# Performance work log

Hardware: AMD Instinct MI355X
Metric: run time of the kernel (lower is better)

## Reference

```python
import jax, jax.numpy as jnp
import numpy as np

D = 512
H = 8
HD = D // H
EPS = 1e-5
NEG_INF = -1e30


def _ln(x, g, b):
    mu = jnp.mean(x, axis=-1, keepdims=True)
    var = jnp.mean(jnp.square(x - mu), axis=-1, keepdims=True)
    return (x - mu) * jax.lax.rsqrt(var + EPS) * g + b


def setup_inputs() -> dict:
    key = jax.random.key(0)
    ks = jax.random.split(key, 8)
    V, M, S = 128, 128, 514  # seq includes 2 head tokens (cls+dist)
    inp = {
        "video_embeds": jax.random.normal(ks[0], (V, D), jnp.float32),
        "music_features": jax.random.normal(ks[1], (M, S, D), jnp.float32),
        "music_masks": jnp.ones((M, S - 2), jnp.int32),
    }
    wk = jax.random.split(ks[2], 5)
    for name, k in zip(["Wq", "Wk", "Wv", "Wo", "Wl"], wk):
        inp[name] = jax.random.normal(k, (D, D), jnp.float32) * 0.02
    for name in ["bq", "bk", "bv", "bo", "bl"]:
        inp[name] = jnp.zeros((D,), jnp.float32)
    for name in ["g1", "g2", "g3"]:
        inp[name] = jnp.ones((D,), jnp.float32)
    for name in ["b1", "b2", "b3"]:
        inp[name] = jnp.zeros((D,), jnp.float32)
    return inp


def reference(video_embeds, music_features, music_masks,
              Wq, bq, Wk, bk, Wv, bv, Wo, bo, Wl, bl,
              g1, b1, g2, b2, g3, b3):
    # drop cls + dist tokens
    mf = music_features[:, 2:, :]  # (M, f, D)
    ve = _ln(video_embeds, g1, b1)  # (V, D)
    mf = _ln(mf, g1, b1)
    V = ve.shape[0]
    M, f, _ = mf.shape

    q = (ve @ Wq.T + bq).reshape(V, H, HD).transpose(1, 0, 2)        # (H, V, hd)
    k = (mf @ Wk.T + bk).reshape(M, f, H, HD).transpose(0, 2, 1, 3)  # (M, H, f, hd)
    v = (mf @ Wv.T + bv).reshape(M, f, H, HD).transpose(0, 2, 1, 3)  # (M, H, f, hd)

    logits = jnp.einsum('hvd,mhfd->vmhf', q, k) / np.sqrt(HD).astype(np.float32)
    mask = music_masks[None, :, None, :]  # (1, M, 1, f)
    logits = jnp.where(mask == 0, NEG_INF, logits)
    w = jax.nn.softmax(logits, axis=-1)
    attn = jnp.einsum('vmhf,mhfd->vmhd', w, v).reshape(V, M, D)
    attn = attn @ Wo.T + bo

    attn = _ln(attn, g2, b2)
    out = attn + (attn @ Wl.T + bl)  # dropout = identity in eval
    return _ln(out, g3, b3)
```

## Files before the change

kernel.cpp:

```cpp
#include <hip/hip_runtime.h>
#include <hip/hip_bf16.h>

typedef unsigned int uint;
typedef unsigned short ushort;
typedef __bf16 bf16;
typedef bf16 bf16x8 __attribute__((ext_vector_type(8)));
typedef float f32x4 __attribute__((ext_vector_type(4)));
typedef ushort ushort4v __attribute__((ext_vector_type(4)));

__device__ __forceinline__ float bf2f(ushort u) {
  union { uint u; float f; } v; v.u = ((uint)u) << 16; return v.f;
}
__device__ __forceinline__ ushort f2bf(float f) {
  union { float f; uint u; } v; v.f = f;
  uint u = v.u;
  uint r = (u + 0x7fffu + ((u >> 16) & 1u)) >> 16;
  return (ushort)r;
}

__device__ __forceinline__ void gl2lds16(const void* g, void* l) {
  __builtin_amdgcn_global_load_lds(
      (const __attribute__((address_space(1))) void*)g,
      (__attribute__((address_space(3))) void*)l, 16, 0, 0);
}

struct CastArgs {
  const float* s0; const float* s1; const float* s2; const float* s3; const float* s4;
  ushort* d0; ushort* d1; ushort* d2; ushort* d3; ushort* d4;
};
__global__ __launch_bounds__(256) void bfcast5(CastArgs a) {
  int t = blockIdx.x * 256 + threadIdx.x;
  int which = t >> 15;
  int e = (t & 32767) * 8;
  const float* s = which == 0 ? a.s0 : which == 1 ? a.s1 : which == 2 ? a.s2 : which == 3 ? a.s3 : a.s4;
  ushort*      d = which == 0 ? a.d0 : which == 1 ? a.d1 : which == 2 ? a.d2 : which == 3 ? a.d3 : a.d4;
  float4 v0 = *(const float4*)(s + e);
  float4 v1 = *(const float4*)(s + e + 4);
  uint4 o;
  o.x = (uint)f2bf(v0.x) | ((uint)f2bf(v0.y) << 16);
  o.y = (uint)f2bf(v0.z) | ((uint)f2bf(v0.w) << 16);
  o.z = (uint)f2bf(v1.x) | ((uint)f2bf(v1.y) << 16);
  o.w = (uint)f2bf(v1.z) | ((uint)f2bf(v1.w) << 16);
  *(uint4*)(d + e) = o;
}

__global__ __launch_bounds__(256) void ln512v(
    int mode, int nrows,
    const void* __restrict__ srcA, const void* __restrict__ srcB,
    const float* __restrict__ g, const float* __restrict__ b,
    void* __restrict__ dst)
{
  const int l = threadIdx.x & 63;
  const int nw = gridDim.x * 4;
  for (int row = blockIdx.x * 4 + (threadIdx.x >> 6); row < nrows; row += nw) {
    float x[8];
    if (mode <= 1) {
      const float* s;
      if (mode == 0) {
        s = (const float*)srcA + (size_t)row * 512;
      } else {
        int mm = row >> 9, fi = row & 511;
        s = (const float*)srcA + ((size_t)mm * 514 + 2 + fi) * 512;
      }
      float4 a0 = *(const float4*)(s + l * 4);
      float4 a1 = *(const float4*)(s + 256 + l * 4);
      x[0] = a0.x; x[1] = a0.y; x[2] = a0.z; x[3] = a0.w;
      x[4] = a1.x; x[5] = a1.y; x[6] = a1.z; x[7] = a1.w;
    } else if (mode == 2) {
      const ushort* s = (const ushort*)srcA + (size_t)row * 512;
      uint4 u = *(const uint4*)(s + l * 8);
      x[0] = bf2f((ushort)u.x); x[1] = bf2f((ushort)(u.x >> 16));
      x[2] = bf2f((ushort)u.y); x[3] = bf2f((ushort)(u.y >> 16));
      x[4] = bf2f((ushort)u.z); x[5] = bf2f((ushort)(u.z >> 16));
      x[6] = bf2f((ushort)u.w); x[7] = bf2f((ushort)(u.w >> 16));
    } else {
      const ushort* sa = (const ushort*)srcA + (size_t)row * 512;
      const ushort* sb = (const ushort*)srcB + (size_t)row * 512;
      uint4 ua = *(const uint4*)(sa + l * 8);
      uint4 ub = *(const uint4*)(sb + l * 8);
      x[0] = bf2f((ushort)ua.x) + bf2f((ushort)ub.x);
      x[1] = bf2f((ushort)(ua.x >> 16)) + bf2f((ushort)(ub.x >> 16));
      x[2] = bf2f((ushort)ua.y) + bf2f((ushort)ub.y);
      x[3] = bf2f((ushort)(ua.y >> 16)) + bf2f((ushort)(ub.y >> 16));
      x[4] = bf2f((ushort)ua.z) + bf2f((ushort)ub.z);
      x[5] = bf2f((ushort)(ua.z >> 16)) + bf2f((ushort)(ub.z >> 16));
      x[6] = bf2f((ushort)ua.w) + bf2f((ushort)ub.w);
      x[7] = bf2f((ushort)(ua.w >> 16)) + bf2f((ushort)(ub.w >> 16));
    }
    float sum = 0.f, sq = 0.f;
    #pragma unroll
    for (int j = 0; j < 8; ++j) { sum += x[j]; sq += x[j] * x[j]; }
    #pragma unroll
    for (int o = 1; o < 64; o <<= 1) {
      sum += __shfl_xor(sum, o);
      sq  += __shfl_xor(sq, o);
    }
    const float inv = 1.f / 512.f;
    float mu = sum * inv;
    float var = sq * inv - mu * mu;
    float rstd = rsqrtf(var + 1e-5f);

    float gv[8], bv[8];
    if (mode <= 1) {
      float4 g0 = *(const float4*)(g + l * 4);
      float4 g1 = *(const float4*)(g + 256 + l * 4);
      float4 b0 = *(const float4*)(b + l * 4);
      float4 b1 = *(const float4*)(b + 256 + l * 4);
      gv[0] = g0.x; gv[1] = g0.y; gv[2] = g0.z; gv[3] = g0.w;
      gv[4] = g1.x; gv[5] = g1.y; gv[6] = g1.z; gv[7] = g1.w;
      bv[0] = b0.x; bv[1] = b0.y; bv[2] = b0.z; bv[3] = b0.w;
      bv[4] = b1.x; bv[5] = b1.y; bv[6] = b1.z; bv[7] = b1.w;
    } else {
      float4 g0 = *(const float4*)(g + l * 8);
      float4 g1 = *(const float4*)(g + l * 8 + 4);
      float4 b0 = *(const float4*)(b + l * 8);
      float4 b1 = *(const float4*)(b + l * 8 + 4);
      gv[0] = g0.x; gv[1] = g0.y; gv[2] = g0.z; gv[3] = g0.w;
      gv[4] = g1.x; gv[5] = g1.y; gv[6] = g1.z; gv[7] = g1.w;
      bv[0] = b0.x; bv[1] = b0.y; bv[2] = b0.z; bv[3] = b0.w;
      bv[4] = b1.x; bv[5] = b1.y; bv[6] = b1.z; bv[7] = b1.w;
    }
    float y[8];
    #pragma unroll
    for (int j = 0; j < 8; ++j) y[j] = (x[j] - mu) * rstd * gv[j] + bv[j];

    if (mode <= 1) {
      ushort* d = (ushort*)dst + (size_t)row * 512;
      ushort4v p0, p1;
      #pragma unroll
      for (int j = 0; j < 4; ++j) { p0[j] = f2bf(y[j]); p1[j] = f2bf(y[4 + j]); }
      *(ushort4v*)(d + l * 4) = p0;
      *(ushort4v*)(d + 256 + l * 4) = p1;
    } else if (mode == 2) {
      ushort* d = (ushort*)dst + (size_t)row * 512;
      uint4 o;
      o.x = (uint)f2bf(y[0]) | ((uint)f2bf(y[1]) << 16);
      o.y = (uint)f2bf(y[2]) | ((uint)f2bf(y[3]) << 16);
      o.z = (uint)f2bf(y[4]) | ((uint)f2bf(y[5]) << 16);
      o.w = (uint)f2bf(y[6]) | ((uint)f2bf(y[7]) << 16);
      *(uint4*)(d + l * 8) = o;
    } else {
      float* d = (float*)dst + (size_t)row * 512;
      float4 o0, o1;
      o0.x = y[0]; o0.y = y[1]; o0.z = y[2]; o0.w = y[3];
      o1.x = y[4]; o1.y = y[5]; o1.z = y[6]; o1.w = y[7];
      *(float4*)(d + l * 8) = o0;
      *(float4*)(d + l * 8 + 4) = o1;
    }
  }
}

__global__ __launch_bounds__(512) void gemm512x(
    const ushort* __restrict__ A, const ushort* __restrict__ W,
    const float* __restrict__ bias, ushort* __restrict__ C,
    float scale, int vt_mode)
{
  __shared__ __align__(16) ushort As[128 * 64];
  __shared__ __align__(16) ushort Bs[256 * 64];
  const int tid = threadIdx.x;
  const int w = tid >> 6, l = tid & 63;
  const int lg = l >> 4, lr = l & 15;
  const int wr = w >> 2, wc = w & 3;

  int nwg = gridDim.x * gridDim.y;
  int bid = blockIdx.y * gridDim.x + blockIdx.x;
  if ((nwg & 7) == 0) bid = (bid & 7) * (nwg >> 3) + (bid >> 3);
  const int bx = bid % gridDim.x, by = bid / gridDim.x;
  const int row0 = by * 128, col0 = bx * 256;

  f32x4 acc[4][4];
  #pragma unroll
  for (int i = 0; i < 4; i++)
    #pragma unroll
    for (int j = 0; j < 4; j++) { f32x4 z = {0.f,0.f,0.f,0.f}; acc[i][j] = z; }

  for (int kk = 0; kk < 8; ++kk) {
    #pragma unroll
    for (int li = 0; li < 2; ++li) {
      int c = li * 512 + tid;
      int r = c >> 3, j = c & 7;
      gl2lds16(A + (size_t)(row0 + r) * 512 + kk * 64 + ((j ^ (r & 7)) * 8),
               As + (li * 512 + w * 64) * 8);
    }
    #pragma unroll
    for (int li = 0; li < 4; ++li) {
      int c = li * 512 + tid;
      int r = c >> 3, j = c & 7;
      gl2lds16(W + (size_t)(col0 + r) * 512 + kk * 64 + ((j ^ (r & 7)) * 8),
               Bs + (li * 512 + w * 64) * 8);
    }
    __syncthreads();
    #pragma unroll
    for (int ks = 0; ks < 2; ++ks) {
      bf16x8 af[4], bfr[4];
      #pragma unroll
      for (int mi = 0; mi < 4; ++mi) {
        int r = wr * 64 + mi * 16 + lr;
        af[mi] = *(const bf16x8*)(As + r * 64 + ((ks * 32 + lg * 8) ^ ((r & 7) * 8)));
      }
      #pragma unroll
      for (int ni = 0; ni < 4; ++ni) {
        int r = wc * 64 + ni * 16 + lr;
        bfr[ni] = *(const bf16x8*)(Bs + r * 64 + ((ks * 32 + lg * 8) ^ ((r & 7) * 8)));
      }
      #pragma unroll
      for (int mi = 0; mi < 4; ++mi)
        #pragma unroll
        for (int ni = 0; ni < 4; ++ni)
          acc[mi][ni] = __builtin_amdgcn_mfma_f32_16x16x32_bf16(af[mi], bfr[ni], acc[mi][ni], 0, 0, 0);
    }
    __syncthreads();
  }

  #pragma unroll
  for (int ni = 0; ni < 4; ++ni) {
    int cg = col0 + wc * 64 + ni * 16 + lr;
    float bc = bias[cg];
    #pragma unroll
    for (int mi = 0; mi < 4; ++mi) {
      int rg0 = row0 + wr * 64 + mi * 16 + lg * 4;
      if (!vt_mode) {
        #pragma unroll
        for (int e = 0; e < 4; ++e) {
          float v = (acc[mi][ni][e] + bc) * scale;
          C[(size_t)(rg0 + e) * 512 + cg] = f2bf(v);
        }
      } else {
        int m = rg0 >> 9, fi = rg0 & 511;
        ushort4v pk;
        #pragma unroll
        for (int e = 0; e < 4; ++e) pk[e] = f2bf((acc[mi][ni][e] + bc) * scale);
        *(ushort4v*)(C + (size_t)(m * 512 + cg) * 512 + fi) = pk;
      }
    }
  }
}

__global__ __launch_bounds__(256) void attn_kernel(
    const ushort* __restrict__ q, const ushort* __restrict__ k,
    const ushort* __restrict__ vt, const int* __restrict__ masks,
    ushort* __restrict__ attn)
{
  __shared__ __align__(16) ushort Qs[128 * 64];
  __shared__ __align__(16) ushort Ks[64 * 64];
  __shared__ __align__(16) ushort Vs[64 * 64];
  __shared__ __align__(16) ushort Ps[4][32 * 64];
  __shared__ float maskf[64];
  __shared__ float stats[4][32];

  const int tid = threadIdx.x;
  const int w = tid >> 6, l = tid & 63;
  const int lg = l >> 4, lr = l & 15;
  const int m = blockIdx.x >> 3, h = blockIdx.x & 7;

  const size_t kbase = (size_t)(m * 512) * 512 + h * 64;
  const size_t vbase = (size_t)(m * 512 + h * 64) * 512;

  #pragma unroll
  for (int c2 = 0; c2 < 4; ++c2) {
    int c = c2 * 256 + tid;
    int r = c >> 3, j = c & 7;
    gl2lds16(q + (size_t)r * 512 + h * 64 + ((j * 8) ^ ((r & 7) * 8)),
             Qs + (c2 * 256 + w * 64) * 8);
  }

  f32x4 acc[2][4];
  #pragma unroll
  for (int i = 0; i < 2; i++)
    #pragma unroll
    for (int j = 0; j < 4; j++) { f32x4 z = {0.f,0.f,0.f,0.f}; acc[i][j] = z; }
  float m_run[2] = {-INFINITY, -INFINITY};
  float l_run[2] = {0.f, 0.f};
  bf16x8 qf[2][2];

  for (int it = 0; it < 8; ++it) {
    const int f0 = it * 64;
    #pragma unroll
    for (int c2 = 0; c2 < 2; ++c2) {
      int c = c2 * 256 + tid;
      int r = c >> 3, j = c & 7;
      int off = (j * 8) ^ ((r & 7) * 8);
      gl2lds16(k + kbase + (size_t)(f0 + r) * 512 + off, Ks + (c2 * 256 + w * 64) * 8);
      gl2lds16(vt + vbase + (size_t)r * 512 + f0 + off, Vs + (c2 * 256 + w * 64) * 8);
    }
    if (tid < 64) maskf[tid] = masks[m * 512 + f0 + tid] ? 0.f : -1e30f;
    __syncthreads();

    if (it == 0) {
      #pragma unroll
      for (int nv = 0; nv < 2; ++nv)
        #pragma unroll
        for (int k2 = 0; k2 < 2; ++k2) {
          int v = w * 32 + nv * 16 + lr;
          qf[nv][k2] = *(const bf16x8*)(Qs + v * 64 + ((k2 * 32 + lg * 8) ^ ((v & 7) * 8)));
        }
    }

    f32x4 s[4][2];
    #pragma unroll
    for (int mi = 0; mi < 4; mi++)
      #pragma unroll
      for (int nv = 0; nv < 2; nv++) { f32x4 z = {0.f,0.f,0.f,0.f}; s[mi][nv] = z; }
    #pragma unroll
    for (int k2 = 0; k2 < 2; ++k2) {
      bf16x8 kf[4];
      #pragma unroll
      for (int mi = 0; mi < 4; ++mi) {
        int f = mi * 16 + lr;
        kf[mi] = *(const bf16x8*)(Ks + f * 64 + ((k2 * 32 + lg * 8) ^ ((f & 7) * 8)));
      }
      #pragma unroll
      for (int mi = 0; mi < 4; ++mi)
        #pragma unroll
        for (int nv = 0; nv < 2; ++nv)
          s[mi][nv] = __builtin_amdgcn_mfma_f32_16x16x32_bf16(kf[mi], qf[nv][k2], s[mi][nv], 0, 0, 0);
    }

    float mk[4][4];
    #pragma unroll
    for (int mi = 0; mi < 4; mi++)
      #pragma unroll
      for (int e = 0; e < 4; e++) mk[mi][e] = maskf[mi * 16 + lg * 4 + e];

    #pragma unroll
    for (int nv = 0; nv < 2; ++nv) {
      float cmax = -INFINITY;
      #pragma unroll
      for (int mi = 0; mi < 4; mi++)
        #pragma unroll
        for (int e = 0; e < 4; e++) {
          s[mi][nv][e] += mk[mi][e];
          cmax = fmaxf(cmax, s[mi][nv][e]);
        }
      cmax = fmaxf(cmax, __shfl_xor(cmax, 16));
      cmax = fmaxf(cmax, __shfl_xor(cmax, 32));
      float mnew = fmaxf(m_run[nv], cmax);
      float sc = __expf(m_run[nv] - mnew);
      float csum = 0.f;
      int vloc = nv * 16 + lr;
      #pragma unroll
      for (int mi = 0; mi < 4; mi++) {
        ushort4v pk;
        #pragma unroll
        for (int e = 0; e < 4; e++) {
          float p = __expf(s[mi][nv][e] - mnew);
          csum += p;
          pk[e] = f2bf(p);
        }
        int f = mi * 16 + lg * 4;
        *(ushort4v*)(&Ps[w][vloc * 64 + (f ^ ((vloc & 7) * 8))]) = pk;
      }
      csum += __shfl_xor(csum, 16);
      csum += __shfl_xor(csum, 32);
      l_run[nv] = l_run[nv] * sc + csum;
      m_run[nv] = mnew;
      if (lg == 0) stats[w][vloc] = sc;
    }

    #pragma unroll
    for (int mi2 = 0; mi2 < 2; ++mi2)
      #pragma unroll
      for (int e = 0; e < 4; ++e) {
        float sc = stats[w][mi2 * 16 + lg * 4 + e];
        #pragma unroll
        for (int nd = 0; nd < 4; ++nd) acc[mi2][nd][e] *= sc;
      }

    #pragma unroll
    for (int k2 = 0; k2 < 2; ++k2) {
      bf16x8 pf[2], vf[4];
      #pragma unroll
      for (int mi2 = 0; mi2 < 2; ++mi2) {
        int vloc = mi2 * 16 + lr;
        pf[mi2] = *(const bf16x8*)(&Ps[w][vloc * 64 + ((k2 * 32 + lg * 8) ^ ((vloc & 7) * 8))]);
      }
      #pragma unroll
      for (int nd = 0; nd < 4; ++nd) {
        int d = nd * 16 + lr;
        vf[nd] = *(const bf16x8*)(Vs + d * 64 + ((k2 * 32 + lg * 8) ^ ((d & 7) * 8)));
      }
      #pragma unroll
      for (int mi2 = 0; mi2 < 2; ++mi2)
        #pragma unroll
        for (int nd = 0; nd < 4; ++nd)
          acc[mi2][nd] = __builtin_amdgcn_mfma_f32_16x16x32_bf16(pf[mi2], vf[nd], acc[mi2][nd], 0, 0, 0);
    }
    __syncthreads();
  }

  #pragma unroll
  for (int nv = 0; nv < 2; ++nv)
    if (lg == 0) stats[w][nv * 16 + lr] = 1.f / l_run[nv];
  #pragma unroll
  for (int mi2 = 0; mi2 < 2; ++mi2)
    #pragma unroll
    for (int e = 0; e < 4; ++e) {
      float invl = stats[w][mi2 * 16 + lg * 4 + e];
      int vg = w * 32 + mi2 * 16 + lg * 4 + e;
      #pragma unroll
      for (int nd = 0; nd < 4; ++nd) {
        int d = nd * 16 + lr;
        attn[(size_t)(vg * 128 + m) * 512 + h * 64 + d] = f2bf(acc[mi2][nd][e] * invl);
      }
    }
}

extern "C" void kernel_launch(void* const* d_in, const int* in_sizes, int n_in,
                              void* d_out, int out_size, void* d_ws, size_t ws_size,
                              hipStream_t stream) {
  const float* video = (const float*)d_in[0];
  const float* music = (const float*)d_in[1];
  const int*   masks = (const int*)d_in[2];
  const float* Wq = (const float*)d_in[3];
  const float* Wk = (const float*)d_in[4];
  const float* Wv = (const float*)d_in[5];
  const float* Wo = (const float*)d_in[6];
  const float* Wl = (const float*)d_in[7];
  const float* bq = (const float*)d_in[8];
  const float* bk = (const float*)d_in[9];
  const float* bv = (const float*)d_in[10];
  const float* bo = (const float*)d_in[11];
  const float* bl = (const float*)d_in[12];
  const float* g1 = (const float*)d_in[13];
  const float* g2 = (const float*)d_in[14];
  const float* g3 = (const float*)d_in[15];
  const float* b1 = (const float*)d_in[16];
  const float* b2 = (const float*)d_in[17];
  const float* b3 = (const float*)d_in[18];

  char* ws = (char*)d_ws;
  ushort* mfln = (ushort*)(ws);
  ushort* kbuf = (ushort*)(ws + 67108864);
  ushort* vtb  = (ushort*)(ws + 134217728);
  ushort* attn = (ushort*)(ws + 201326592);
  ushort* c1   = (ushort*)(ws + 218103808);
  ushort* xbuf = (ushort*)(ws + 234881024);
  ushort* veln = (ushort*)(ws + 251658240);
  ushort* qbuf = (ushort*)(ws + 251789312);
  ushort* wqb  = (ushort*)(ws + 251920384);
  ushort* wkb  = wqb + 262144;
  ushort* wvb  = wkb + 262144;
  ushort* wob  = wvb + 262144;
  ushort* wlb  = wob + 262144;

  CastArgs ca = {Wq, Wk, Wv, Wo, Wl, wqb, wkb, wvb, wob, wlb};
  bfcast5<<<640, 256, 0, stream>>>(ca);

  ln512v<<<32, 256, 0, stream>>>(0, 128, video, nullptr, g1, b1, veln);
  ln512v<<<2048, 256, 0, stream>>>(1, 65536, music, nullptr, g1, b1, mfln);

  gemm512x<<<dim3(2, 1), 512, 0, stream>>>(veln, wqb, bq, qbuf, 0.125f, 0);
  gemm512x<<<dim3(2, 512), 512, 0, stream>>>(mfln, wkb, bk, kbuf, 1.f, 0);
  gemm512x<<<dim3(2, 512), 512, 0, stream>>>(mfln, wvb, bv, vtb, 1.f, 1);

  attn_kernel<<<1024, 256, 0, stream>>>(qbuf, kbuf, vtb, masks, attn);

  gemm512x<<<dim3(2, 128), 512, 0, stream>>>(attn, wob, bo, c1, 1.f, 0);
  ln512v<<<2048, 256, 0, stream>>>(2, 16384, c1, nullptr, g2, b2, xbuf);
  gemm512x<<<dim3(2, 128), 512, 0, stream>>>(xbuf, wlb, bl, c1, 1.f, 0);
  ln512v<<<2048, 256, 0, stream>>>(3, 16384, xbuf, c1, g3, b3, d_out);
}
```

Before: 309.3 us.

## Fuse preamble kernels and compute K, V, Q projections in one GEMM

Merges the weight cast and both input LayerNorms into a single preamble launch. Replaces the separate Q, K and V GEMM launches with one kernel that computes K and V from a shared A tile, so the music activations are loaded once for both projections, and handles Q in an extra row of blocks. Adds s_setprio around the MFMA blocks in all GEMM and attention loops to favour matrix issue. The fused kernel uses a 128x128 tile with 256 threads, which holds more accumulators per thread and may lower occupancy. The preamble relies on the cast, video LN and music LN blocks being independent of each other, which they are.

After: 313.9 us. Within noise of the previous version (+1.5%).

```diff
diff --git a/kernel.cpp b/kernel.cpp
--- a/kernel.cpp
+++ b/kernel.cpp
@@ -24,35 +24,15 @@
       (__attribute__((address_space(3))) void*)l, 16, 0, 0);
 }
 
-struct CastArgs {
-  const float* s0; const float* s1; const float* s2; const float* s3; const float* s4;
-  ushort* d0; ushort* d1; ushort* d2; ushort* d3; ushort* d4;
-};
-__global__ __launch_bounds__(256) void bfcast5(CastArgs a) {
-  int t = blockIdx.x * 256 + threadIdx.x;
-  int which = t >> 15;
-  int e = (t & 32767) * 8;
-  const float* s = which == 0 ? a.s0 : which == 1 ? a.s1 : which == 2 ? a.s2 : which == 3 ? a.s3 : a.s4;
-  ushort*      d = which == 0 ? a.d0 : which == 1 ? a.d1 : which == 2 ? a.d2 : which == 3 ? a.d3 : a.d4;
-  float4 v0 = *(const float4*)(s + e);
-  float4 v1 = *(const float4*)(s + e + 4);
-  uint4 o;
-  o.x = (uint)f2bf(v0.x) | ((uint)f2bf(v0.y) << 16);
-  o.y = (uint)f2bf(v0.z) | ((uint)f2bf(v0.w) << 16);
-  o.z = (uint)f2bf(v1.x) | ((uint)f2bf(v1.y) << 16);
-  o.w = (uint)f2bf(v1.z) | ((uint)f2bf(v1.w) << 16);
-  *(uint4*)(d + e) = o;
-}
-
-__global__ __launch_bounds__(256) void ln512v(
-    int mode, int nrows,
+__device__ __forceinline__ void ln_rows(
+    int mode, int nrows, int blk, int nblk, int tid,
     const void* __restrict__ srcA, const void* __restrict__ srcB,
     const float* __restrict__ g, const float* __restrict__ b,
     void* __restrict__ dst)
 {
-  const int l = threadIdx.x & 63;
-  const int nw = gridDim.x * 4;
-  for (int row = blockIdx.x * 4 + (threadIdx.x >> 6); row < nrows; row += nw) {
+  const int l = tid & 63;
+  const int nw = nblk * 4;
+  for (int row = blk * 4 + (tid >> 6); row < nrows; row += nw) {
     float x[8];
     if (mode <= 1) {
       const float* s;
@@ -150,6 +130,152 @@
   }
 }
 
+__global__ __launch_bounds__(256) void ln512v(
+    int mode, int nrows,
+    const void* __restrict__ srcA, const void* __restrict__ srcB,
+    const float* __restrict__ g, const float* __restrict__ b,
+    void* __restrict__ dst)
+{
+  ln_rows(mode, nrows, blockIdx.x, gridDim.x, threadIdx.x, srcA, srcB, g, b, dst);
+}
+
+struct PreArgs {
+  const float* s0; const float* s1; const float* s2; const float* s3; const float* s4;
+  ushort* d0; ushort* d1; ushort* d2; ushort* d3; ushort* d4;
+  const float* video; const float* music;
+  const float* g1; const float* b1;
+  ushort* veln; ushort* mfln;
+};
+__global__ __launch_bounds__(256) void preamble(PreArgs a) {
+  int bb = blockIdx.x;
+  if (bb < 640) {
+    int t = bb * 256 + threadIdx.x;
+    int which = t >> 15;
+    int e = (t & 32767) * 8;
+    const float* s = which == 0 ? a.s0 : which == 1 ? a.s1 : which == 2 ? a.s2 : which == 3 ? a.s3 : a.s4;
+    ushort*      d = which == 0 ? a.d0 : which == 1 ? a.d1 : which == 2 ? a.d2 : which == 3 ? a.d3 : a.d4;
+    float4 v0 = *(const float4*)(s + e);
+    float4 v1 = *(const float4*)(s + e + 4);
+    uint4 o;
+    o.x = (uint)f2bf(v0.x) | ((uint)f2bf(v0.y) << 16);
+    o.y = (uint)f2bf(v0.z) | ((uint)f2bf(v0.w) << 16);
+    o.z = (uint)f2bf(v1.x) | ((uint)f2bf(v1.y) << 16);
+    o.w = (uint)f2bf(v1.z) | ((uint)f2bf(v1.w) << 16);
+    *(uint4*)(d + e) = o;
+  } else if (bb < 672) {
+    ln_rows(0, 128, bb - 640, 32, threadIdx.x, a.video, nullptr, a.g1, a.b1, a.veln);
+  } else {
+    ln_rows(1, 65536, bb - 672, 2048, threadIdx.x, a.music, nullptr, a.g1, a.b1, a.mfln);
+  }
+}
+
+__global__ __launch_bounds__(256) void gemm_kvq(
+    const ushort* __restrict__ A, const ushort* __restrict__ Aq,
+    const ushort* __restrict__ Wk, const ushort* __restrict__ Wv,
+    const ushort* __restrict__ Wq,
+    const float* __restrict__ bk, const float* __restrict__ bv,
+    const float* __restrict__ bq,
+    ushort* __restrict__ K, ushort* __restrict__ Vt, ushort* __restrict__ Q)
+{
+  __shared__ __align__(16) ushort As[128 * 64];
+  __shared__ __align__(16) ushort Bks[128 * 64];
+  __shared__ __align__(16) ushort Bvs[128 * 64];
+  const int tid = threadIdx.x;
+  const int w = tid >> 6, l = tid & 63;
+  const int lg = l >> 4, lr = l & 15;
+  const int wr = w >> 1, wc = w & 1;
+  const bool isq = (blockIdx.y == 512);
+  const int row0 = isq ? 0 : blockIdx.y * 128;
+  const int col0 = blockIdx.x * 128;
+  const ushort* Ap  = isq ? Aq : A;
+  const ushort* Wkp = isq ? Wq : Wk;
+
+  f32x4 kacc[4][4], vacc[4][4];
+  #pragma unroll
+  for (int i = 0; i < 4; i++)
+    #pragma unroll
+    for (int j = 0; j < 4; j++) {
+      f32x4 z = {0.f,0.f,0.f,0.f};
+      kacc[i][j] = z; vacc[i][j] = z;
+    }
+
+  for (int kk = 0; kk < 8; ++kk) {
+    #pragma unroll
+    for (int c2 = 0; c2 < 4; ++c2) {
+      int c = c2 * 256 + tid;
+      int r = c >> 3, j = c & 7;
+      int ksrc = kk * 64 + ((j ^ (r & 7)) * 8);
+      int dst = (c2 * 256 + w * 64) * 8;
+      gl2lds16(Ap  + (size_t)(row0 + r) * 512 + ksrc, As  + dst);
+      gl2lds16(Wkp + (size_t)(col0 + r) * 512 + ksrc, Bks + dst);
+      if (!isq) gl2lds16(Wv + (size_t)(col0 + r) * 512 + ksrc, Bvs + dst);
+    }
+    __syncthreads();
+    #pragma unroll
+    for (int ks = 0; ks < 2; ++ks) {
+      bf16x8 af[4], bkf[4];
+      #pragma unroll
+      for (int mi = 0; mi < 4; ++mi) {
+        int r = wr * 64 + mi * 16 + lr;
+        af[mi] = *(const bf16x8*)(As + r * 64 + ((ks * 32 + lg * 8) ^ ((r & 7) * 8)));
+      }
+      #pragma unroll
+      for (int ni = 0; ni < 4; ++ni) {
+        int r = wc * 64 + ni * 16 + lr;
+        bkf[ni] = *(const bf16x8*)(Bks + r * 64 + ((ks * 32 + lg * 8) ^ ((r & 7) * 8)));
+      }
+      __builtin_amdgcn_s_setprio(1);
+      #pragma unroll
+      for (int mi = 0; mi < 4; ++mi)
+        #pragma unroll
+        for (int ni = 0; ni < 4; ++ni)
+          kacc[mi][ni] = __builtin_amdgcn_mfma_f32_16x16x32_bf16(af[mi], bkf[ni], kacc[mi][ni], 0, 0, 0);
+      __builtin_amdgcn_s_setprio(0);
+      if (!isq) {
+        bf16x8 bvf[4];
+        #pragma unroll
+        for (int ni = 0; ni < 4; ++ni) {
+          int r = wc * 64 + ni * 16 + lr;
+          bvf[ni] = *(const bf16x8*)(Bvs + r * 64 + ((ks * 32 + lg * 8) ^ ((r & 7) * 8)));
+        }
+        __builtin_amdgcn_s_setprio(1);
+        #pragma unroll
+        for (int mi = 0; mi < 4; ++mi)
+          #pragma unroll
+          for (int ni = 0; ni < 4; ++ni)
+            vacc[mi][ni] = __builtin_amdgcn_mfma_f32_16x16x32_bf16(af[mi], bvf[ni], vacc[mi][ni], 0, 0, 0);
+        __builtin_amdgcn_s_setprio(0);
+      }
+    }
+    __syncthreads();
+  }
+
+  #pragma unroll
+  for (int ni = 0; ni < 4; ++ni) {
+    int cg = col0 + wc * 64 + ni * 16 + lr;
+    float bkc = isq ? bq[cg] : bk[cg];
+    float bvc = isq ? 0.f : bv[cg];
+    #pragma unroll
+    for (int mi = 0; mi < 4; ++mi) {
+      int rg0 = row0 + wr * 64 + mi * 16 + lg * 4;
+      if (isq) {
+        #pragma unroll
+        for (int e = 0; e < 4; ++e)
+          Q[(size_t)(rg0 + e) * 512 + cg] = f2bf((kacc[mi][ni][e] + bkc) * 0.125f);
+      } else {
+        #pragma unroll
+        for (int e = 0; e < 4; ++e)
+          K[(size_t)(rg0 + e) * 512 + cg] = f2bf(kacc[mi][ni][e] + bkc);
+        int m = rg0 >> 9, fi = rg0 & 511;
+        ushort4v pk;
+        #pragma unroll
+        for (int e = 0; e < 4; ++e) pk[e] = f2bf(vacc[mi][ni][e] + bvc);
+        *(ushort4v*)(Vt + (size_t)(m * 512 + cg) * 512 + fi) = pk;
+      }
+    }
+  }
+}
+
 __global__ __launch_bounds__(512) void gemm512x(
     const ushort* __restrict__ A, const ushort* __restrict__ W,
     const float* __restrict__ bias, ushort* __restrict__ C,
@@ -203,11 +329,13 @@
         int r = wc * 64 + ni * 16 + lr;
         bfr[ni] = *(const bf16x8*)(Bs + r * 64 + ((ks * 32 + lg * 8) ^ ((r & 7) * 8)));
       }
+      __builtin_amdgcn_s_setprio(1);
       #pragma unroll
       for (int mi = 0; mi < 4; ++mi)
         #pragma unroll
         for (int ni = 0; ni < 4; ++ni)
           acc[mi][ni] = __builtin_amdgcn_mfma_f32_16x16x32_bf16(af[mi], bfr[ni], acc[mi][ni], 0, 0, 0);
+      __builtin_amdgcn_s_setprio(0);
     }
     __syncthreads();
   }
@@ -309,11 +437,13 @@
         int f = mi * 16 + lr;
         kf[mi] = *(const bf16x8*)(Ks + f * 64 + ((k2 * 32 + lg * 8) ^ ((f & 7) * 8)));
       }
+      __builtin_amdgcn_s_setprio(1);
       #pragma unroll
       for (int mi = 0; mi < 4; ++mi)
         #pragma unroll
         for (int nv = 0; nv < 2; ++nv)
           s[mi][nv] = __builtin_amdgcn_mfma_f32_16x16x32_bf16(kf[mi], qf[nv][k2], s[mi][nv], 0, 0, 0);
+      __builtin_amdgcn_s_setprio(0);
     }
 
     float mk[4][4];
@@ -379,11 +509,13 @@
         int d = nd * 16 + lr;
         vf[nd] = *(const bf16x8*)(Vs + d * 64 + ((k2 * 32 + lg * 8) ^ ((d & 7) * 8)));
       }
+      __builtin_amdgcn_s_setprio(1);
       #pragma unroll
       for (int mi2 = 0; mi2 < 2; ++mi2)
         #pragma unroll
         for (int nd = 0; nd < 4; ++nd)
           acc[mi2][nd] = __builtin_amdgcn_mfma_f32_16x16x32_bf16(pf[mi2], vf[nd], acc[mi2][nd], 0, 0, 0);
+      __builtin_amdgcn_s_setprio(0);
     }
     __syncthreads();
   }
@@ -443,15 +575,12 @@
   ushort* wob  = wvb + 262144;
   ushort* wlb  = wob + 262144;
 
-  CastArgs ca = {Wq, Wk, Wv, Wo, Wl, wqb, wkb, wvb, wob, wlb};
-  bfcast5<<<640, 256, 0, stream>>>(ca);
-
-  ln512v<<<32, 256, 0, stream>>>(0, 128, video, nullptr, g1, b1, veln);
-  ln512v<<<2048, 256, 0, stream>>>(1, 65536, music, nullptr, g1, b1, mfln);
-
-  gemm512x<<<dim3(2, 1), 512, 0, stream>>>(veln, wqb, bq, qbuf, 0.125f, 0);
-  gemm512x<<<dim3(2, 512), 512, 0, stream>>>(mfln, wkb, bk, kbuf, 1.f, 0);
-  gemm512x<<<dim3(2, 512), 512, 0, stream>>>(mfln, wvb, bv, vtb, 1.f, 1);
+  PreArgs pa = {Wq, Wk, Wv, Wo, Wl, wqb, wkb, wvb, wob, wlb,
+                video, music, g1, b1, veln, mfln};
+  preamble<<<2720, 256, 0, stream>>>(pa);
+
+  gemm_kvq<<<dim3(4, 513), 256, 0, stream>>>(
+      mfln, veln, wkb, wvb, wqb, bk, bv, bq, kbuf, vtb, qbuf);
 
   attn_kernel<<<1024, 256, 0, stream>>>(qbuf, kbuf, vtb, masks, attn);
 
```
